# Kernel tuning notes

Hardware: AMD Instinct MI355X
Metric: run time of the kernel (lower is better)

## Reference

```python
import jax, jax.numpy as jnp
import numpy as np

# Dimensions (TinyLlama-like)
B, T = 4, 1024
D = 2048          # hidden_size
H, DH = 32, 64    # heads, head_dim
HK = 8            # kv heads (GQA, n_rep = 4)
RQ, RKV = 32, 32  # per-head SVD ranks
RO, RF = 1024, 1024
I = 5632          # intermediate_size
THETA = 10000.0
EPS = 1e-5


def setup_inputs() -> dict:
    key = jax.random.key(0)
    ks = jax.random.split(key, 16)
    p = lambda k, s: jax.random.normal(k, s, jnp.float32) * 0.02
    return {
        "x": jax.random.normal(ks[0], (B, T, D), jnp.float32),
        "ln1_w": jnp.ones((D,), jnp.float32),
        "ln2_w": jnp.ones((D,), jnp.float32),
        "q_Us": p(ks[1], (H, DH, RQ)),  "q_V": p(ks[2], (H, RQ, D)),
        "k_Us": p(ks[3], (HK, DH, RKV)), "k_V": p(ks[4], (HK, RKV, D)),
        "v_Us": p(ks[5], (HK, DH, RKV)), "v_V": p(ks[6], (HK, RKV, D)),
        "o_Us": p(ks[7], (D, RO)),  "o_V": p(ks[8], (RO, H * DH)),
        "g_Us": p(ks[9], (I, RF)),  "g_V": p(ks[10], (RF, D)),
        "u_Us": p(ks[11], (I, RF)), "u_V": p(ks[12], (RF, D)),
        "d_Us": p(ks[13], (D, RF)), "d_V": p(ks[14], (RF, I)),
    }


def _rms(x, w):
    return x * jax.lax.rsqrt(jnp.mean(x * x, axis=-1, keepdims=True) + EPS) * w


def _rope_cos_sin(t_len, dh, dtype):
    half = dh // 2
    inv_freq = 1.0 / (THETA ** (jnp.arange(half, dtype=jnp.float32) / half))
    ang = jnp.arange(t_len, dtype=jnp.float32)[:, None] * inv_freq[None, :]  # [T, half]
    return jnp.cos(ang).astype(dtype), jnp.sin(ang).astype(dtype)


def _apply_rope(x, cos, sin):
    # x: [B,h,T,Dh], LLaMA half-split rotation
    half = x.shape[-1] // 2
    x1, x2 = x[..., :half], x[..., half:]
    c = cos[None, None]  # [1,1,T,half]
    s = sin[None, None]
    return jnp.concatenate([x1 * c - x2 * s, x2 * c + x1 * s], axis=-1)


def reference(x, ln1_w, ln2_w, q_Us, q_V, k_Us, k_V, v_Us, v_V,
              o_Us, o_V, g_Us, g_V, u_Us, u_V, d_Us, d_V):
    b, t, d = x.shape
    h1 = _rms(x, ln1_w)

    # per-head low-rank projections: y_h = x @ V_h^T @ Us_h^T
    q = jnp.einsum('bhtr,hdr->bhtd', jnp.einsum('btD,hrD->bhtr', h1, q_V), q_Us)  # [B,H,T,Dh]
    k = jnp.einsum('bhtr,hdr->bhtd', jnp.einsum('btD,hrD->bhtr', h1, k_V), k_Us)  # [B,Hk,T,Dh]
    v = jnp.einsum('bhtr,hdr->bhtd', jnp.einsum('btD,hrD->bhtr', h1, v_V), v_Us)

    cos, sin = _rope_cos_sin(t, DH, x.dtype)
    q = _apply_rope(q, cos, sin)
    k = _apply_rope(k, cos, sin)

    n_rep = H // HK
    k = jnp.repeat(k, n_rep, axis=1)  # _repeat_kv
    v = jnp.repeat(v, n_rep, axis=1)

    scale = 1.0 / np.sqrt(DH)
    scores = jnp.einsum('bhtd,bhsd->bhts', q, k) * scale
    causal = jnp.tril(jnp.ones((t, t), bool))
    scores = jnp.where(causal[None, None], scores, jnp.finfo(scores.dtype).min)
    attn = jax.nn.softmax(scores, axis=-1)
    ctx = jnp.einsum('bhts,bhsd->bhtd', attn, v)
    ctx = ctx.transpose(0, 2, 1, 3).reshape(b, t, H * DH)

    # low-rank output proj: o = ctx @ o_V^T @ o_Us^T
    attn_out = jnp.einsum('btr,Dr->btD', jnp.einsum('btk,rk->btr', ctx, o_V), o_Us)
    x = x + attn_out

    # SwiGLU MLP with low-rank factors
    h2 = _rms(x, ln2_w)
    g = jnp.einsum('btr,ir->bti', jnp.einsum('btD,rD->btr', h2, g_V), g_Us)
    u = jnp.einsum('btr,ir->bti', jnp.einsum('btD,rD->btr', h2, u_V), u_Us)
    ff = jax.nn.silu(g) * u
    down = jnp.einsum('btr,Dr->btD', jnp.einsum('bti,ri->btr', ff, d_V), d_Us)
    return x + down
```

## Files before the change

kernel.cpp:

```cpp
#include <hip/hip_runtime.h>
#include <math.h>

typedef unsigned short u16;
typedef unsigned int u32;
typedef __bf16 bf16x8 __attribute__((ext_vector_type(8)));
typedef float f32x4 __attribute__((ext_vector_type(4)));

__device__ __forceinline__ float bf2f(u16 u) {
  union { u32 i; float f; } x; x.i = ((u32)u) << 16; return x.f;
}
__device__ __forceinline__ u16 f2bf(float f) {
  union { float f; u32 i; } x; x.f = f;
  return (u16)((x.i + 0x7fffu + ((x.i >> 16) & 1u)) >> 16);
}

#define GLDS16(gp, lp)                                                        \
  __builtin_amdgcn_global_load_lds(                                           \
      (const __attribute__((address_space(1))) u32*)(gp),                     \
      (__attribute__((address_space(3))) u32*)(lp), 16, 0, 0)

__global__ void detect_k(const u16* __restrict__ w, int* __restrict__ flag) {
  if (threadIdx.x == 0 && blockIdx.x == 0)
    *flag = (w[0] == 0x0000u && w[1] == 0x3F80u) ? 1 : 0;
}

__global__ __launch_bounds__(256) void rope_tab_k(float2* __restrict__ tab) {
  const int idx = blockIdx.x * 256 + threadIdx.x;
  const int t = idx >> 5, j = idx & 31;
  float inv = powf(10000.0f, -(float)j * (1.0f / 32.0f));
  float ang = (float)t * inv;
  float sn, cs;
  sincosf(ang, &sn, &cs);
  tab[idx] = make_float2(cs, sn);
}

struct CvtArgs {
  const void* src[17];
  u32 dstOff[17];
  u32 blkOff[18];
};

__global__ __launch_bounds__(256) void cvt_all(CvtArgs a, u16* __restrict__ dstB,
                                               const int* __restrict__ flag,
                                               const void* __restrict__ w1src,
                                               u16* __restrict__ h1) {
  int seg = 0;
  const int bx = blockIdx.x;
#pragma unroll 1
  while (bx >= (int)a.blkOff[seg + 1]) seg++;
  const int tid = threadIdx.x;
  const long local = ((long)(bx - a.blkOff[seg]) * 256 + tid) * 8;
  u16* dst = dstB + a.dstOff[seg] + local;
  const bool f32in = (*flag != 0);
  uint4 o; u16* op = (u16*)&o;
  if (f32in) {
    const float* s = (const float*)a.src[seg] + local;
    float4 va = *(const float4*)(s);
    float4 vb = *(const float4*)(s + 4);
    op[0] = f2bf(va.x); op[1] = f2bf(va.y); op[2] = f2bf(va.z); op[3] = f2bf(va.w);
    op[4] = f2bf(vb.x); op[5] = f2bf(vb.y); op[6] = f2bf(vb.z); op[7] = f2bf(vb.w);
  } else {
    o = *(const uint4*)((const u16*)a.src[seg] + local);
  }
  *(uint4*)dst = o;

  if (seg == 0) {
    float v[8];
    float ss = 0.f;
#pragma unroll
    for (int i = 0; i < 8; i++) { v[i] = bf2f(op[i]); ss += v[i] * v[i]; }
#pragma unroll
    for (int off = 32; off > 0; off >>= 1) ss += __shfl_xor(ss, off);
    __shared__ float red[4];
    if ((tid & 63) == 0) red[tid >> 6] = ss;
    __syncthreads();
    const float total = red[0] + red[1] + red[2] + red[3];
    const float inv = rsqrtf(total * (1.0f / 2048.0f) + 1e-5f);
    float wv[8];
    if (f32in) {
      const float* wp = (const float*)w1src + tid * 8;
      float4 wa = *(const float4*)(wp);
      float4 wb = *(const float4*)(wp + 4);
      wv[0] = bf2f(f2bf(wa.x)); wv[1] = bf2f(f2bf(wa.y));
      wv[2] = bf2f(f2bf(wa.z)); wv[3] = bf2f(f2bf(wa.w));
      wv[4] = bf2f(f2bf(wb.x)); wv[5] = bf2f(f2bf(wb.y));
      wv[6] = bf2f(f2bf(wb.z)); wv[7] = bf2f(f2bf(wb.w));
    } else {
      uint4 ww = *((const uint4*)w1src + tid);
      const u16* wp = (const u16*)&ww;
#pragma unroll
      for (int i = 0; i < 8; i++) wv[i] = bf2f(wp[i]);
    }
    uint4 ho; u16* hop = (u16*)&ho;
#pragma unroll
    for (int i = 0; i < 8; i++) hop[i] = f2bf(v[i] * inv * wv[i]);
    *(uint4*)(h1 + (long)bx * 2048 + tid * 8) = ho;
  }
}

__global__ __launch_bounds__(256) void rms_k(const u16* __restrict__ x,
                                             const u16* __restrict__ w,
                                             u16* __restrict__ out) {
  const long row = blockIdx.x;
  const u16* xr = x + row * 2048;
  u16* orow = out + row * 2048;
  const int tid = threadIdx.x;
  const int base = tid * 8;
  uint4 u = *(const uint4*)(xr + base);
  const u16* us = (const u16*)&u;
  float v[8];
  float ss = 0.f;
#pragma unroll
  for (int i = 0; i < 8; i++) { v[i] = bf2f(us[i]); ss += v[i] * v[i]; }
#pragma unroll
  for (int off = 32; off > 0; off >>= 1) ss += __shfl_xor(ss, off);
  __shared__ float red[4];
  if ((tid & 63) == 0) red[tid >> 6] = ss;
  __syncthreads();
  float total = red[0] + red[1] + red[2] + red[3];
  float inv = rsqrtf(total * (1.0f / 2048.0f) + 1e-5f);
  uint4 wv = *(const uint4*)(w + base);
  const u16* wp = (const u16*)&wv;
  uint4 o;
  u16* op = (u16*)&o;
#pragma unroll
  for (int i = 0; i < 8; i++) op[i] = f2bf(v[i] * inv * bf2f(wp[i]));
  *(uint4*)(orow + base) = o;
}

template <int EPI>
__global__ __launch_bounds__(256, 3) void gemm_bt(const u16* __restrict__ A,
                                                  const u16* __restrict__ B,
                                                  void* Cv,
                                                  void* Cv2,
                                                  const u16* R,
                                                  const int* flagp,
                                                  int N, int Klen, int lda, int ldb) {
  __shared__ u16 As[128 * 32];
  __shared__ u16 Bs[128 * 32];
  const long koff = (long)blockIdx.z * Klen;
  A += koff;
  B += koff;
  if (blockIdx.z) Cv = Cv2;
  const int m0 = blockIdx.y * 128;
  const int n0 = blockIdx.x * 128;
  const int tid = threadIdx.x;
  const int wave = tid >> 6;
  const int lane = tid & 63;
  const int wr = (wave >> 1) * 64;
  const int wc = (wave & 1) * 64;
  const int l16 = lane & 15;
  const int quad = lane >> 4;
  u16* C = (u16*)Cv;
  float* Cf = (float*)Cv;
  bool f32o = false;
  if (EPI == 3) f32o = (*flagp != 0);

  f32x4 acc[4][4];
#pragma unroll
  for (int i = 0; i < 4; i++)
#pragma unroll
    for (int j = 0; j < 4; j++) acc[i][j] = (f32x4){0.f, 0.f, 0.f, 0.f};

  const int srow = wave * 16 + (lane >> 2);
  const int scol = (lane & 3) * 8;
  const u16* Ag = A + (long)(m0 + srow) * lda + scol;
  const u16* Bg = B + (long)(n0 + srow) * ldb + scol;
  const long astep = (long)64 * lda;
  const long bstep = (long)64 * ldb;
  u16* Asw = &As[wave * 16 * 32];
  u16* Bsw = &Bs[wave * 16 * 32];

  for (int k0 = 0; k0 < Klen; k0 += 32) {
    GLDS16(Ag + k0, Asw);
    GLDS16(Ag + astep + k0, Asw + 64 * 32);
    GLDS16(Bg + k0, Bsw);
    GLDS16(Bg + bstep + k0, Bsw + 64 * 32);
    __syncthreads();
    bf16x8 af[4], bfr[4];
#pragma unroll
    for (int t = 0; t < 4; t++) {
      af[t]  = *(const bf16x8*)(&As[(wr + t * 16 + l16) * 32 + quad * 8]);
      bfr[t] = *(const bf16x8*)(&Bs[(wc + t * 16 + l16) * 32 + quad * 8]);
    }
#pragma unroll
    for (int i = 0; i < 4; i++)
#pragma unroll
      for (int j = 0; j < 4; j++)
        acc[i][j] = __builtin_amdgcn_mfma_f32_16x16x32_bf16(bfr[j], af[i], acc[i][j], 0, 0, 0);
    __syncthreads();
  }

#pragma unroll
  for (int i = 0; i < 4; i++) {
    const int m = m0 + wr + i * 16 + l16;
#pragma unroll
    for (int j = 0; j < 4; j++) {
      const int n = n0 + wc + j * 16 + quad * 4;
      const long idx = (long)m * N + n;
      float v[4];
#pragma unroll
      for (int r = 0; r < 4; r++) v[r] = acc[i][j][r];
      if (EPI == 1 || EPI == 3) {
        uint2 rr = *(const uint2*)(R + idx);
        const u16* rp = (const u16*)&rr;
#pragma unroll
        for (int r = 0; r < 4; r++) v[r] += bf2f(rp[r]);
      }
      if (EPI == 3 && f32o) {
        float4 o = {v[0], v[1], v[2], v[3]};
        *(float4*)(Cf + idx) = o;
      } else {
        uint2 o; u16* op = (u16*)&o;
#pragma unroll
        for (int r = 0; r < 4; r++) op[r] = f2bf(v[r]);
        *(uint2*)(C + idx) = o;
      }
    }
  }
}

#define STAGE_SILU(buf, k0)                                                   \
  do {                                                                        \
    GLDS16(Ag_ + (k0), &SH[buf][0][woff]);                                    \
    GLDS16(Au_ + (k0), &SH[buf][1][woff]);                                    \
    GLDS16(Bg_ + (k0), &SH[buf][2][woff]);                                    \
    GLDS16(Bu_ + (k0), &SH[buf][3][woff]);                                    \
  } while (0)

__global__ __launch_bounds__(512, 4) void gemm_silu(const u16* __restrict__ Agp,
                                                    const u16* __restrict__ Aup,
                                                    const u16* __restrict__ Bgp,
                                                    const u16* __restrict__ Bup,
                                                    u16* __restrict__ C,
                                                    int N, int Klen, int lda, int ldb) {
  __shared__ u16 SH[2][4][128 * 32];
  const int m0 = blockIdx.y * 128;
  const int n0 = blockIdx.x * 128;
  const int tid = threadIdx.x;
  const int wave = tid >> 6;
  const int lane = tid & 63;
  const int wid = wave & 3;
  const int isU = wave >> 2;
  const int wr = (wid >> 1) * 64;
  const int wc = (wid & 1) * 64;
  const int l16 = lane & 15;
  const int quad = lane >> 4;
  const int matA = isU;
  const int matB = 2 + isU;

  f32x4 acc[4][4];
#pragma unroll
  for (int i = 0; i < 4; i++)
#pragma unroll
    for (int j = 0; j < 4; j++) acc[i][j] = (f32x4){0.f, 0.f, 0.f, 0.f};

  const int srow = wave * 16 + (lane >> 2);
  const int scol = ((lane & 3) ^ ((lane >> 3) & 3)) * 8;
  const u16* Ag_ = Agp + (long)(m0 + srow) * lda + scol;
  const u16* Au_ = Aup + (long)(m0 + srow) * lda + scol;
  const u16* Bg_ = Bgp + (long)(n0 + srow) * ldb + scol;
  const u16* Bu_ = Bup + (long)(n0 + srow) * ldb + scol;
  const int woff = wave * 512;
  const int rsw = (quad ^ ((l16 >> 1) & 3)) * 8;

  const int nk = Klen >> 5;
  STAGE_SILU(0, 0);
  int cur = 0;
  for (int kt = 0; kt < nk; ++kt) {
    if (kt + 1 < nk) {
      STAGE_SILU(cur ^ 1, (kt + 1) << 5);
      asm volatile("s_waitcnt vmcnt(4)" ::: "memory");
    } else {
      asm volatile("s_waitcnt vmcnt(0)" ::: "memory");
    }
    asm volatile("s_barrier" ::: "memory");
    bf16x8 af[4], bfr[4];
#pragma unroll
    for (int t = 0; t < 4; t++) {
      af[t]  = *(const bf16x8*)(&SH[cur][matA][(wr + t * 16 + l16) * 32 + rsw]);
      bfr[t] = *(const bf16x8*)(&SH[cur][matB][(wc + t * 16 + l16) * 32 + rsw]);
    }
#pragma unroll
    for (int i = 0; i < 4; i++)
#pragma unroll
      for (int j = 0; j < 4; j++)
        acc[i][j] = __builtin_amdgcn_mfma_f32_16x16x32_bf16(bfr[j], af[i], acc[i][j], 0, 0, 0);
    asm volatile("s_barrier" ::: "memory");
    cur ^= 1;
  }

  float* xch = (float*)&SH[0][0][0];
  if (isU) {
    float* w = xch + wid * 4096 + lane * 4;
#pragma unroll
    for (int i = 0; i < 4; i++)
#pragma unroll
      for (int j = 0; j < 4; j++)
        *(f32x4*)(w + (i * 4 + j) * 256) = acc[i][j];
  }
  __syncthreads();
  if (!isU) {
    const float* w = xch + wid * 4096 + lane * 4;
#pragma unroll
    for (int i = 0; i < 4; i++) {
      const int m = m0 + wr + i * 16 + l16;
#pragma unroll
      for (int j = 0; j < 4; j++) {
        const int n = n0 + wc + j * 16 + quad * 4;
        const long idx = (long)m * N + n;
        f32x4 uv = *(const f32x4*)(w + (i * 4 + j) * 256);
        uint2 o; u16* op = (u16*)&o;
#pragma unroll
        for (int r = 0; r < 4; r++) {
          float g = acc[i][j][r];
          float v = uv[r] * g / (1.f + __expf(-g));
          op[r] = f2bf(v);
        }
        *(uint2*)(C + idx) = o;
      }
    }
  }
}

__global__ __launch_bounds__(256) void combine2(const u16* __restrict__ a,
                                                const u16* __restrict__ b,
                                                u16* __restrict__ o) {
  const long i = ((long)blockIdx.x * 256 + threadIdx.x) * 8;
  uint4 ua = *(const uint4*)(a + i);
  uint4 ub = *(const uint4*)(b + i);
  const u16* pa = (const u16*)&ua;
  const u16* pb = (const u16*)&ub;
  uint4 uo; u16* po = (u16*)&uo;
#pragma unroll
  for (int j = 0; j < 8; j++) po[j] = f2bf(bf2f(pa[j]) + bf2f(pb[j]));
  *(uint4*)(o + i) = uo;
}

__global__ __launch_bounds__(256) void expand_k(const u16* __restrict__ rbuf,
                                                int rstride,
                                                const u16* __restrict__ Us,
                                                u16* __restrict__ out,
                                                const float2* __restrict__ tab,
                                                int nheads, int doRope) {
  const int tok = blockIdx.x;
  const int wave = threadIdx.x >> 6;
  const int d = threadIdx.x & 63;
  const int h = blockIdx.y * 4 + wave;
  const int b = tok >> 10;
  const int t = tok & 1023;
  const u16* up = Us + ((long)h * 64 + d) * 32;
  const u16* rp = rbuf + (long)tok * rstride + h * 32;
  float s = 0.f;
#pragma unroll
  for (int c = 0; c < 4; c++) {
    uint4 uu = *(const uint4*)(up + c * 8);
    uint4 rr = *(const uint4*)(rp + c * 8);
    const u16* u8p = (const u16*)&uu;
    const u16* r8p = (const u16*)&rr;
#pragma unroll
    for (int i = 0; i < 8; i++) s += bf2f(u8p[i]) * bf2f(r8p[i]);
  }
  if (doRope) {
    const int j = d & 31;
    float2 cs2 = tab[(t << 5) | j];
    float partner = __shfl_xor(s, 32);
    s = (d < 32) ? (s * cs2.x - partner * cs2.y) : (s * cs2.x + partner * cs2.y);
  }
  out[(((long)(b * nheads + h)) * 1024 + t) * 64 + d] = f2bf(s);
}

__global__ __launch_bounds__(256) void vT_k(const u16* __restrict__ vbuf,
                                            u16* __restrict__ vT) {
  __shared__ u16 tile[64][72];
  const int b = blockIdx.z, kh = blockIdx.y;
  const int t0 = blockIdx.x * 64;
  const int tid = threadIdx.x;
  const int r = tid >> 2;
  const int c = (tid & 3) * 16;
  const u16* src = vbuf + ((long)(b * 8 + kh) * 1024 + t0 + r) * 64 + c;
  *(uint4*)&tile[r][c] = *(const uint4*)src;
  *(uint4*)&tile[r][c + 8] = *(const uint4*)(src + 8);
  __syncthreads();
  u16 tmp[16];
#pragma unroll
  for (int i = 0; i < 16; i++) tmp[i] = tile[c + i][r];
  u16* dst = vT + ((long)(b * 8 + kh) * 64 + r) * 1024 + t0 + c;
  *(uint4*)dst = *(uint4*)&tmp[0];
  *(uint4*)(dst + 8) = *(uint4*)&tmp[8];
}

#define ATS 72

__global__ __launch_bounds__(256, 2) void attn_mfma(const u16* __restrict__ q,
                                                    const u16* __restrict__ k,
                                                    const u16* __restrict__ vT,
                                                    u16* __restrict__ ctx) {
  __shared__ u16 Ks[64 * ATS];
  __shared__ u16 Vts[64 * ATS];
  __shared__ u16 Plds[4][16 * ATS];
  const int bx = blockIdx.x;
  const int h = blockIdx.y;
  const int b = blockIdx.z;
  const int kh = h >> 2;
  const int qlo = bx * 64;
  const int qhi = (15 - bx) * 64;
  const int tid = threadIdx.x;
  const int wave = tid >> 6;
  const int lane = tid & 63;
  const int l16 = lane & 15;
  const int quad = lane >> 4;

  const u16* qb = q + ((long)(b * 32 + h) * 1024) * 64;
  const u16* kb = k + ((long)(b * 8 + kh) * 1024) * 64;
  const u16* vb = vT + ((long)(b * 8 + kh) * 64) * 1024;

  bf16x8 qfl[2], qfh[2];
  {
    const u16* qp = qb + (long)(qlo + wave * 16 + l16) * 64 + quad * 8;
    qfl[0] = *(const bf16x8*)(qp);
    qfl[1] = *(const bf16x8*)(qp + 32);
    qp = qb + (long)(qhi + wave * 16 + l16) * 64 + quad * 8;
    qfh[0] = *(const bf16x8*)(qp);
    qfh[1] = *(const bf16x8*)(qp + 32);
  }

  float ml[4], ll[4], mh[4], lh[4];
  f32x4 ol[4], oh[4];
#pragma unroll
  for (int r = 0; r < 4; r++) { ml[r] = -1e30f; ll[r] = 0.f; mh[r] = -1e30f; lh[r] = 0.f; }
#pragma unroll
  for (int j = 0; j < 4; j++) { ol[j] = (f32x4){0.f, 0.f, 0.f, 0.f}; oh[j] = ol[j]; }

  const int srow = tid >> 2;
  const int sc0 = (tid & 3) * 16;
  int s0 = 0;

  auto process = [&](const bf16x8* qf, float* m, float* l, f32x4* oacc, int qtb) {
    f32x4 s[4];
#pragma unroll
    for (int t = 0; t < 4; t++) {
      s[t] = (f32x4){0.f, 0.f, 0.f, 0.f};
      const u16* kr = &Ks[(t * 16 + l16) * ATS + quad * 8];
      bf16x8 b0 = *(const bf16x8*)(kr);
      bf16x8 b1 = *(const bf16x8*)(kr + 32);
      s[t] = __builtin_amdgcn_mfma_f32_16x16x32_bf16(qf[0], b0, s[t], 0, 0, 0);
      s[t] = __builtin_amdgcn_mfma_f32_16x16x32_bf16(qf[1], b1, s[t], 0, 0, 0);
    }
#pragma unroll
    for (int t = 0; t < 4; t++) s[t] *= 0.125f;
    if (s0 == qtb) {
#pragma unroll
      for (int t = 0; t < 4; t++)
#pragma unroll
        for (int r = 0; r < 4; r++)
          if (s0 + t * 16 + l16 > qtb + wave * 16 + quad * 4 + r) s[t][r] = -1e30f;
    }
    float p[4][4];
#pragma unroll
    for (int r = 0; r < 4; r++) {
      float mx = fmaxf(fmaxf(s[0][r], s[1][r]), fmaxf(s[2][r], s[3][r]));
#pragma unroll
      for (int off = 1; off < 16; off <<= 1) mx = fmaxf(mx, __shfl_xor(mx, off));
      const float mnew = fmaxf(m[r], mx);
      const float alpha = __expf(m[r] - mnew);
      float ps = 0.f;
#pragma unroll
      for (int t = 0; t < 4; t++) { p[t][r] = __expf(s[t][r] - mnew); ps += p[t][r]; }
#pragma unroll
      for (int off = 1; off < 16; off <<= 1) ps += __shfl_xor(ps, off);
      l[r] = l[r] * alpha + ps;
      m[r] = mnew;
#pragma unroll
      for (int j = 0; j < 4; j++) oacc[j][r] *= alpha;
    }
    u16* pw = &Plds[wave][0];
#pragma unroll
    for (int t = 0; t < 4; t++)
#pragma unroll
      for (int r = 0; r < 4; r++)
        pw[(quad * 4 + r) * ATS + t * 16 + l16] = f2bf(p[t][r]);
    bf16x8 pf0 = *(const bf16x8*)(&pw[l16 * ATS + quad * 8]);
    bf16x8 pf1 = *(const bf16x8*)(&pw[l16 * ATS + 32 + quad * 8]);
#pragma unroll
    for (int j = 0; j < 4; j++) {
      const u16* vr = &Vts[(j * 16 + l16) * ATS + quad * 8];
      bf16x8 v0 = *(const bf16x8*)(vr);
      bf16x8 v1 = *(const bf16x8*)(vr + 32);
      oacc[j] = __builtin_amdgcn_mfma_f32_16x16x32_bf16(pf0, v0, oacc[j], 0, 0, 0);
      oacc[j] = __builtin_amdgcn_mfma_f32_16x16x32_bf16(pf1, v1, oacc[j], 0, 0, 0);
    }
  };

  for (s0 = 0; s0 <= qhi; s0 += 64) {
    __syncthreads();
    {
      const u16* kp = kb + (long)(s0 + srow) * 64 + sc0;
      *(uint4*)&Ks[srow * ATS + sc0] = *(const uint4*)kp;
      *(uint4*)&Ks[srow * ATS + sc0 + 8] = *(const uint4*)(kp + 8);
      const u16* vp = vb + (long)srow * 1024 + s0 + sc0;
      *(uint4*)&Vts[srow * ATS + sc0] = *(const uint4*)vp;
      *(uint4*)&Vts[srow * ATS + sc0 + 8] = *(const uint4*)(vp + 8);
    }
    __syncthreads();
    process(qfh, mh, lh, oh, qhi);
    if (s0 <= qlo) process(qfl, ml, ll, ol, qlo);
  }

#pragma unroll
  for (int r = 0; r < 4; r++) {
    const int rowl = qlo + wave * 16 + quad * 4 + r;
    const int rowh = qhi + wave * 16 + quad * 4 + r;
    const float il = 1.f / ll[r];
    const float ih = 1.f / lh[r];
#pragma unroll
    for (int j = 0; j < 4; j++) {
      ctx[(((long)(b * 1024 + rowl)) * 32 + h) * 64 + j * 16 + l16] = f2bf(ol[j][r] * il);
      ctx[(((long)(b * 1024 + rowh)) * 32 + h) * 64 + j * 16 + l16] = f2bf(oh[j][r] * ih);
    }
  }
}

extern "C" void kernel_launch(void* const* d_in, const int* in_sizes, int n_in,
                              void* d_out, int out_size, void* d_ws, size_t ws_size,
                              hipStream_t stream) {
  char* ws = (char*)d_ws;
  u16* cb = (u16*)ws;
  u16* cx    = cb + 0;
  u16* cln1  = cb + 8388608;
  u16* cln2  = cb + 8390656;
  u16* cqUs  = cb + 8392704;
  u16* ckUs  = cb + 8458240;
  u16* cvUs  = cb + 8474624;
  u16* cqkvV = cb + 8491008;
  u16* coUs  = cb + 11636736;
  u16* coV   = cb + 13733888;
  u16* cguV  = cb + 15831040;
  u16* cgUs  = cb + 20025344;
  u16* cuUs  = cb + 25792512;
  u16* cdUs  = cb + 31559680;
  u16* cdV   = cb + 33656832;

  char* P = ws + 78848000;
  u16* h1    = (u16*)(P + 0);
  u16* qkvr  = (u16*)(P + 16777216);
  u16* qp0   = (u16*)(P + 33554432);
  u16* qp1   = (u16*)(P + 46137344);
  u16* qbuf  = (u16*)(P + 33554432);
  u16* kbuf  = (u16*)(P + 50331648);
  u16* vbuf  = (u16*)(P + 54525952);
  u16* ctx   = (u16*)(P + 58720256);
  u16* vbufT = (u16*)(P + 75497472);
  u16* orr   = (u16*)(P + 75497472);
  u16* xmid  = (u16*)(P + 83886080);
  u16* op0   = (u16*)(P + 0);
  u16* op1   = (u16*)(P + 8388608);
  u16* h2    = (u16*)(P + 0);
  u16* gur   = (u16*)(P + 16777216);
  u16* gbuf  = (u16*)(P + 33554432);
  u16* dp0   = (u16*)(P + 0);
  u16* dp1   = (u16*)(P + 8388608);
  u16* dr    = (u16*)(P + 16777216);
  float2* ropetab = (float2*)(P + 79691776);
  int* flag  = (int*)(ws + 179511296);

  const dim3 blk(256);
  detect_k<<<1, 64, 0, stream>>>((const u16*)d_in[1], flag);
  rope_tab_k<<<128, blk, 0, stream>>>(ropetab);

  CvtArgs ca;
  const u32 dOff[17] = {0u, 8388608u, 8390656u, 8392704u, 8491008u, 8458240u,
                        10588160u, 8474624u, 11112448u, 11636736u, 13733888u,
                        20025344u, 15831040u, 25792512u, 17928192u, 31559680u,
                        33656832u};
  const u32 nblk[17] = {4096u, 1u, 1u, 32u, 1024u, 8u, 256u, 8u, 256u, 1024u,
                        1024u, 2816u, 1024u, 2816u, 1024u, 1024u, 2816u};
  u32 cum = 0;
  for (int i = 0; i < 17; i++) {
    ca.src[i] = d_in[i];
    ca.dstOff[i] = dOff[i];
    ca.blkOff[i] = cum;
    cum += nblk[i];
  }
  ca.blkOff[17] = cum;
  cvt_all<<<cum, blk, 0, stream>>>(ca, cb, flag, d_in[1], h1);

  gemm_bt<0><<<dim3(12, 32, 2), blk, 0, stream>>>(h1, cqkvV, qp0, qp1, nullptr, nullptr, 1536, 1024, 2048, 2048);
  combine2<<<3072, blk, 0, stream>>>(qp0, qp1, qkvr);
  expand_k<<<dim3(4096, 8), blk, 0, stream>>>(qkvr, 1536, cqUs, qbuf, ropetab, 32, 1);
  expand_k<<<dim3(4096, 2), blk, 0, stream>>>(qkvr + 1024, 1536, ckUs, kbuf, ropetab, 8, 1);
  expand_k<<<dim3(4096, 2), blk, 0, stream>>>(qkvr + 1280, 1536, cvUs, vbuf, ropetab, 8, 0);
  vT_k<<<dim3(16, 8, 4), blk, 0, stream>>>(vbuf, vbufT);
  attn_mfma<<<dim3(8, 32, 4), blk, 0, stream>>>(qbuf, kbuf, vbufT, ctx);
  gemm_bt<0><<<dim3(8, 32, 2), blk, 0, stream>>>(ctx, coV, op0, op1, nullptr, nullptr, 1024, 1024, 2048, 2048);
  combine2<<<2048, blk, 0, stream>>>(op0, op1, orr);
  gemm_bt<1><<<dim3(16, 32), blk, 0, stream>>>(orr, coUs, xmid, nullptr, cx, nullptr, 2048, 1024, 1024, 1024);
  rms_k<<<4096, blk, 0, stream>>>(xmid, cln2, h2);
  gemm_bt<0><<<dim3(16, 32), blk, 0, stream>>>(h2, cguV, gur, nullptr, nullptr, nullptr, 2048, 2048, 2048, 2048);
  gemm_silu<<<dim3(44, 32), dim3(512), 0, stream>>>(gur, gur + 1024, cgUs, cuUs, gbuf, 5632, 1024, 2048, 1024);
  gemm_bt<0><<<dim3(8, 32, 2), blk, 0, stream>>>(gbuf, cdV, dp0, dp1, nullptr, nullptr, 1024, 2816, 5632, 5632);
  combine2<<<2048, blk, 0, stream>>>(dp0, dp1, dr);
  gemm_bt<3><<<dim3(16, 32), blk, 0, stream>>>(dr, cdUs, d_out, nullptr, xmid, flag, 2048, 1024, 1024, 1024);
}
```

Baseline: 768.1 us.

## Fuse split-K combine into QKV expand, prefetch K/V tiles, prioritize attention MFMAs

The split-K partial sums for the QKV low-rank projection are now added inside a single fused expand kernel that handles Q, K and V heads in one launch, replacing one combine pass and three expand launches. The attention kernel gains register prefetching of the next K/V tile during compute, plus s_setprio around its MFMA blocks. Workspace buffers are remapped so K, V and Q no longer overlap the partial buffers that are still being read. The fused kernel reads both partials for every head, so the rank-row reads repeat across the expand blocks, and the prefetch costs extra registers.

```diff
diff --git a/kernel.cpp b/kernel.cpp
--- a/kernel.cpp
+++ b/kernel.cpp
@@ -337,37 +337,54 @@
   *(uint4*)(o + i) = uo;
 }
 
-__global__ __launch_bounds__(256) void expand_k(const u16* __restrict__ rbuf,
-                                                int rstride,
-                                                const u16* __restrict__ Us,
-                                                u16* __restrict__ out,
-                                                const float2* __restrict__ tab,
-                                                int nheads, int doRope) {
+__global__ __launch_bounds__(256) void expand_fused(const u16* __restrict__ p0,
+                                                    const u16* __restrict__ p1,
+                                                    const u16* __restrict__ qUs,
+                                                    const u16* __restrict__ kUs,
+                                                    const u16* __restrict__ vUs,
+                                                    u16* __restrict__ qout,
+                                                    u16* __restrict__ kout,
+                                                    u16* __restrict__ vout,
+                                                    const float2* __restrict__ tab) {
   const int tok = blockIdx.x;
   const int wave = threadIdx.x >> 6;
   const int d = threadIdx.x & 63;
-  const int h = blockIdx.y * 4 + wave;
+  const int y = blockIdx.y;
+  int mode, hbase;
+  if (y < 8)       { mode = 0; hbase = y * 4; }
+  else if (y < 10) { mode = 1; hbase = (y - 8) * 4; }
+  else             { mode = 2; hbase = (y - 10) * 4; }
+  const int h = hbase + wave;
   const int b = tok >> 10;
   const int t = tok & 1023;
+  const int roff = (mode == 0) ? 0 : (mode == 1 ? 1024 : 1280);
+  const u16* Us = (mode == 0) ? qUs : (mode == 1 ? kUs : vUs);
   const u16* up = Us + ((long)h * 64 + d) * 32;
-  const u16* rp = rbuf + (long)tok * rstride + h * 32;
+  const long rbase = (long)tok * 1536 + roff + h * 32;
+  const u16* rp0 = p0 + rbase;
+  const u16* rp1 = p1 + rbase;
   float s = 0.f;
 #pragma unroll
   for (int c = 0; c < 4; c++) {
     uint4 uu = *(const uint4*)(up + c * 8);
-    uint4 rr = *(const uint4*)(rp + c * 8);
+    uint4 r0 = *(const uint4*)(rp0 + c * 8);
+    uint4 r1 = *(const uint4*)(rp1 + c * 8);
     const u16* u8p = (const u16*)&uu;
-    const u16* r8p = (const u16*)&rr;
-#pragma unroll
-    for (int i = 0; i < 8; i++) s += bf2f(u8p[i]) * bf2f(r8p[i]);
-  }
-  if (doRope) {
+    const u16* r0p = (const u16*)&r0;
+    const u16* r1p = (const u16*)&r1;
+#pragma unroll
+    for (int i = 0; i < 8; i++) s += bf2f(u8p[i]) * (bf2f(r0p[i]) + bf2f(r1p[i]));
+  }
+  if (mode < 2) {
     const int j = d & 31;
     float2 cs2 = tab[(t << 5) | j];
     float partner = __shfl_xor(s, 32);
     s = (d < 32) ? (s * cs2.x - partner * cs2.y) : (s * cs2.x + partner * cs2.y);
   }
-  out[(((long)(b * nheads + h)) * 1024 + t) * 64 + d] = f2bf(s);
+  const u16 val = f2bf(s);
+  if (mode == 0)      qout[(((long)(b * 32 + h)) * 1024 + t) * 64 + d] = val;
+  else if (mode == 1) kout[(((long)(b * 8 + h)) * 1024 + t) * 64 + d] = val;
+  else                vout[(((long)(b * 8 + h)) * 1024 + t) * 64 + d] = val;
 }
 
 __global__ __launch_bounds__(256) void vT_k(const u16* __restrict__ vbuf,
@@ -438,6 +455,7 @@
 
   auto process = [&](const bf16x8* qf, float* m, float* l, f32x4* oacc, int qtb) {
     f32x4 s[4];
+    __builtin_amdgcn_s_setprio(1);
 #pragma unroll
     for (int t = 0; t < 4; t++) {
       s[t] = (f32x4){0.f, 0.f, 0.f, 0.f};
@@ -447,6 +465,7 @@
       s[t] = __builtin_amdgcn_mfma_f32_16x16x32_bf16(qf[0], b0, s[t], 0, 0, 0);
       s[t] = __builtin_amdgcn_mfma_f32_16x16x32_bf16(qf[1], b1, s[t], 0, 0, 0);
     }
+    __builtin_amdgcn_s_setprio(0);
 #pragma unroll
     for (int t = 0; t < 4; t++) s[t] *= 0.125f;
     if (s0 == qtb) {
@@ -482,6 +501,7 @@
         pw[(quad * 4 + r) * ATS + t * 16 + l16] = f2bf(p[t][r]);
     bf16x8 pf0 = *(const bf16x8*)(&pw[l16 * ATS + quad * 8]);
     bf16x8 pf1 = *(const bf16x8*)(&pw[l16 * ATS + 32 + quad * 8]);
+    __builtin_amdgcn_s_setprio(1);
 #pragma unroll
     for (int j = 0; j < 4; j++) {
       const u16* vr = &Vts[(j * 16 + l16) * ATS + quad * 8];
@@ -490,19 +510,34 @@
       oacc[j] = __builtin_amdgcn_mfma_f32_16x16x32_bf16(pf0, v0, oacc[j], 0, 0, 0);
       oacc[j] = __builtin_amdgcn_mfma_f32_16x16x32_bf16(pf1, v1, oacc[j], 0, 0, 0);
     }
+    __builtin_amdgcn_s_setprio(0);
   };
+
+  uint4 kA, kB, vA, vB;
+  {
+    const u16* kp = kb + (long)srow * 64 + sc0;
+    kA = *(const uint4*)kp;
+    kB = *(const uint4*)(kp + 8);
+    const u16* vp = vb + (long)srow * 1024 + sc0;
+    vA = *(const uint4*)vp;
+    vB = *(const uint4*)(vp + 8);
+  }
 
   for (s0 = 0; s0 <= qhi; s0 += 64) {
     __syncthreads();
-    {
-      const u16* kp = kb + (long)(s0 + srow) * 64 + sc0;
-      *(uint4*)&Ks[srow * ATS + sc0] = *(const uint4*)kp;
-      *(uint4*)&Ks[srow * ATS + sc0 + 8] = *(const uint4*)(kp + 8);
-      const u16* vp = vb + (long)srow * 1024 + s0 + sc0;
-      *(uint4*)&Vts[srow * ATS + sc0] = *(const uint4*)vp;
-      *(uint4*)&Vts[srow * ATS + sc0 + 8] = *(const uint4*)(vp + 8);
-    }
+    *(uint4*)&Ks[srow * ATS + sc0] = kA;
+    *(uint4*)&Ks[srow * ATS + sc0 + 8] = kB;
+    *(uint4*)&Vts[srow * ATS + sc0] = vA;
+    *(uint4*)&Vts[srow * ATS + sc0 + 8] = vB;
     __syncthreads();
+    if (s0 + 64 <= qhi) {
+      const u16* kp = kb + (long)(s0 + 64 + srow) * 64 + sc0;
+      kA = *(const uint4*)kp;
+      kB = *(const uint4*)(kp + 8);
+      const u16* vp = vb + (long)srow * 1024 + (s0 + 64) + sc0;
+      vA = *(const uint4*)vp;
+      vB = *(const uint4*)(vp + 8);
+    }
     process(qfh, mh, lh, oh, qhi);
     if (s0 <= qlo) process(qfl, ml, ll, ol, qlo);
   }
@@ -527,7 +562,6 @@
   char* ws = (char*)d_ws;
   u16* cb = (u16*)ws;
   u16* cx    = cb + 0;
-  u16* cln1  = cb + 8388608;
   u16* cln2  = cb + 8390656;
   u16* cqUs  = cb + 8392704;
   u16* ckUs  = cb + 8458240;
@@ -543,12 +577,11 @@
 
   char* P = ws + 78848000;
   u16* h1    = (u16*)(P + 0);
-  u16* qkvr  = (u16*)(P + 16777216);
+  u16* kbuf  = (u16*)(P + 0);
+  u16* vbuf  = (u16*)(P + 4194304);
+  u16* qbuf  = (u16*)(P + 16777216);
   u16* qp0   = (u16*)(P + 33554432);
   u16* qp1   = (u16*)(P + 46137344);
-  u16* qbuf  = (u16*)(P + 33554432);
-  u16* kbuf  = (u16*)(P + 50331648);
-  u16* vbuf  = (u16*)(P + 54525952);
   u16* ctx   = (u16*)(P + 58720256);
   u16* vbufT = (u16*)(P + 75497472);
   u16* orr   = (u16*)(P + 75497472);
@@ -586,10 +619,8 @@
   cvt_all<<<cum, blk, 0, stream>>>(ca, cb, flag, d_in[1], h1);
 
   gemm_bt<0><<<dim3(12, 32, 2), blk, 0, stream>>>(h1, cqkvV, qp0, qp1, nullptr, nullptr, 1536, 1024, 2048, 2048);
-  combine2<<<3072, blk, 0, stream>>>(qp0, qp1, qkvr);
-  expand_k<<<dim3(4096, 8), blk, 0, stream>>>(qkvr, 1536, cqUs, qbuf, ropetab, 32, 1);
-  expand_k<<<dim3(4096, 2), blk, 0, stream>>>(qkvr + 1024, 1536, ckUs, kbuf, ropetab, 8, 1);
-  expand_k<<<dim3(4096, 2), blk, 0, stream>>>(qkvr + 1280, 1536, cvUs, vbuf, ropetab, 8, 0);
+  expand_fused<<<dim3(4096, 12), blk, 0, stream>>>(qp0, qp1, cqUs, ckUs, cvUs,
+                                                   qbuf, kbuf, vbuf, ropetab);
   vT_k<<<dim3(16, 8, 4), blk, 0, stream>>>(vbuf, vbufT);
   attn_mfma<<<dim3(8, 32, 4), blk, 0, stream>>>(qbuf, kbuf, vbufT, ctx);
   gemm_bt<0><<<dim3(8, 32, 2), blk, 0, stream>>>(ctx, coV, op0, op1, nullptr, nullptr, 1024, 1024, 2048, 2048);
```

Result: no change. 762.7 us (-0.7%).
